# Kernel optimization log

Measured on AMD Instinct MI355X. Metric: run time of the kernel, lower is better.

The kernel has to match this reference:

```python
import jax, jax.numpy as jnp
import numpy as np

N = 4096
TAU = 0.2          # args.tau relaxation temperature
EPS = 1e-10        # numerical guard for logit of clamped probs


def setup_inputs() -> dict:
    key = jax.random.key(0)
    k1, k2, k3 = jax.random.split(key, 3)
    r = jax.random.uniform(k1, (N, N))
    ori_adj = jnp.where(r < 0.005, -1.0, jnp.where(r < 0.01, 1.0, 0.0)).astype(jnp.float32)
    # nn.init.uniform_(change_links_prob, 0.0, 0.001)
    change_links_prob = jax.random.uniform(k2, (N, N), minval=0.0, maxval=0.001, dtype=jnp.float32)
    # uniform noise for the RelaxedBernoulli logistic reparameterization
    u = jax.random.uniform(k3, (N, N), minval=1e-6, maxval=1.0 - 1e-6, dtype=jnp.float32)
    return {"ori_adj": ori_adj, "change_links_prob": change_links_prob, "u": u}


def reference(ori_adj, change_links_prob, u):
    # --- get_modified_adj: RelaxedBernoulliStraightThrough(tau, clamp(p,0,1)).rsample() ---
    p = jnp.clip(change_links_prob, EPS, 1.0 - EPS)      # torch.clamp(p, 0, 1) + logit guard
    logits = jnp.log(p) - jnp.log1p(-p)
    noise = jnp.log(u) - jnp.log1p(-u)                   # logistic noise
    soft = jax.nn.sigmoid((logits + noise) / TAU)        # relaxed sample
    hard = jnp.round(soft)                               # quantized sample
    change_prob = soft + jax.lax.stop_gradient(hard - soft)  # straight-through
    mod_adj = ori_adj + change_prob * (-2.0 * ori_adj)   # ori_adj * (1 - 2*b)

    # --- balance_degree_directed(mod_adj) ---
    # torch.diag(matrix) returns the diagonal VECTOR, broadcast-subtracted per row (faithful).
    A = mod_adj + mod_adj.T - jnp.diag(mod_adj)
    A_abs = jnp.abs(A)
    tr3 = jnp.einsum('ij,jk,ki->', A, A, A)              # trace(A @ A @ A)
    tr3_abs = jnp.einsum('ij,jk,ki->', A_abs, A_abs, A_abs)
    balance = 0.5 * (1.0 + tr3 / tr3_abs)
    return mod_adj, balance
```

## Files before the change

kernel.cpp:

```cpp
#include <hip/hip_runtime.h>
#include <hip/hip_bf16.h>
#include <cstdint>
#include <cstddef>

#define N 4096
#define NN ((size_t)N * (size_t)N)

typedef int int4v  __attribute__((ext_vector_type(4)));
typedef int int16v __attribute__((ext_vector_type(16)));

__device__ inline void async16(const void* g, void* lds) {
    __builtin_amdgcn_global_load_lds(
        (const __attribute__((address_space(1))) void*)g,
        (__attribute__((address_space(3))) void*)lds, 16, 0, 0);
}

__device__ inline float mod_elem(float p, float uu, float o) {
    p = fminf(fmaxf(p, 1e-10f), 1.0f - 1e-10f);
    float logits = logf(p) - log1pf(-p);
    float noise  = logf(uu) - log1pf(-uu);
    float y = (logits + noise) / 0.2f;
    float soft = 1.0f / (1.0f + expf(-y));
    float hard = rintf(soft);
    return o + hard * (-2.0f * o);
}

__global__ void diag_kernel(const float* __restrict__ ori, const float* __restrict__ clp,
                            const float* __restrict__ u, float* __restrict__ diag,
                            double* __restrict__ accs) {
    int j = blockIdx.x * blockDim.x + threadIdx.x;
    size_t idx = (size_t)j * N + j;
    diag[j] = mod_elem(clp[idx], u[idx], ori[idx]);
    if (blockIdx.x == 0 && threadIdx.x < 2) accs[threadIdx.x] = 0.0;
}

__global__ __launch_bounds__(256) void fused_mod_A(
        const float* __restrict__ ori, const float* __restrict__ clp,
        const float* __restrict__ u, const float* __restrict__ diag,
        float* __restrict__ out,
        signed char* __restrict__ A, signed char* __restrict__ AT,
        signed char* __restrict__ Aa, signed char* __restrict__ ATa) {
    const int bx = blockIdx.x, by = blockIdx.y;
    if (bx > by) return;
    const int bi = bx * 32, bj = by * 32;
    __shared__ float mij[32][33];
    __shared__ float mji[32][33];
    const int t = threadIdx.x;
    const int r  = t >> 3;
    const int c4 = (t & 7) * 4;
    {
        size_t idx = (size_t)(bi + r) * N + bj + c4;
        float4 p4 = *(const float4*)&clp[idx];
        float4 u4 = *(const float4*)&u[idx];
        float4 o4 = *(const float4*)&ori[idx];
        float m0 = mod_elem(p4.x, u4.x, o4.x);
        float m1 = mod_elem(p4.y, u4.y, o4.y);
        float m2 = mod_elem(p4.z, u4.z, o4.z);
        float m3 = mod_elem(p4.w, u4.w, o4.w);
        *(float4*)&out[idx] = make_float4(m0, m1, m2, m3);
        mij[r][c4] = m0; mij[r][c4 + 1] = m1; mij[r][c4 + 2] = m2; mij[r][c4 + 3] = m3;
        if (bx != by) {
            size_t idx2 = (size_t)(bj + r) * N + bi + c4;
            float4 q4 = *(const float4*)&clp[idx2];
            float4 v4 = *(const float4*)&u[idx2];
            float4 w4 = *(const float4*)&ori[idx2];
            float n0 = mod_elem(q4.x, v4.x, w4.x);
            float n1 = mod_elem(q4.y, v4.y, w4.y);
            float n2 = mod_elem(q4.z, v4.z, w4.z);
            float n3 = mod_elem(q4.w, v4.w, w4.w);
            *(float4*)&out[idx2] = make_float4(n0, n1, n2, n3);
            mji[r][c4] = n0; mji[r][c4 + 1] = n1; mji[r][c4 + 2] = n2; mji[r][c4 + 3] = n3;
        } else {
            mji[r][c4] = m0; mji[r][c4 + 1] = m1; mji[r][c4 + 2] = m2; mji[r][c4 + 3] = m3;
        }
    }
    __syncthreads();
    const float djr = diag[bj + r];
    const float dir = diag[bi + r];
    int pkA = 0, pkAa = 0, pkT = 0, pkTa = 0;
    int qkA = 0, qkAa = 0, qkT = 0, qkTa = 0;
    #pragma unroll
    for (int k = 0; k < 4; ++k) {
        const int c = c4 + k;
        const float x = mij[r][c], xt = mij[c][r];
        const float y = mji[r][c], yt = mji[c][r];
        int ai = (int)(x + yt - diag[bj + c]);
        int ti = (int)(xt + y - djr);
        pkA  |= (ai & 255) << (8 * k);
        pkAa |= ((ai < 0 ? -ai : ai) & 255) << (8 * k);
        pkT  |= (ti & 255) << (8 * k);
        pkTa |= ((ti < 0 ? -ti : ti) & 255) << (8 * k);
        int mi = (int)(y + xt - diag[bi + c]);
        int si = (int)(yt + x - dir);
        qkA  |= (mi & 255) << (8 * k);
        qkAa |= ((mi < 0 ? -mi : mi) & 255) << (8 * k);
        qkT  |= (si & 255) << (8 * k);
        qkTa |= ((si < 0 ? -si : si) & 255) << (8 * k);
    }
    const size_t o1 = (size_t)(bi + r) * N + bj + c4;
    const size_t o2 = (size_t)(bj + r) * N + bi + c4;
    *(int*)&A [o1] = pkA;  *(int*)&Aa [o1] = pkAa;
    *(int*)&AT[o2] = pkT;  *(int*)&ATa[o2] = pkTa;
    if (bx != by) {
        *(int*)&A [o2] = qkA;  *(int*)&Aa [o2] = qkAa;
        *(int*)&AT[o1] = qkT;  *(int*)&ATa[o1] = qkTa;
    }
}

__global__ __launch_bounds__(256) void gemm_trace_i8(const signed char* __restrict__ Ag,
                                                     const signed char* __restrict__ ATg,
                                                     const signed char* __restrict__ Aag,
                                                     const signed char* __restrict__ ATag,
                                                     double* __restrict__ accs) {
    __shared__ int4v As4[1024];
    __shared__ int4v Bs4[1024];
    __shared__ int red[4];
    const int z = blockIdx.z;
    const signed char* Asrc = z ? Aag  : Ag;
    const signed char* Bsrc = z ? ATag : ATg;
    const int i0 = blockIdx.y * 128;
    const int k0 = blockIdx.x * 128;
    const int t = threadIdx.x;
    const int lane = t & 63;
    const int wave = t >> 6;
    const int wr = (wave >> 1) * 64;
    const int wc = (wave & 1) * 64;
    const int m32 = lane & 31;
    const int kg  = lane >> 5;
    signed char* Asc = (signed char*)As4;
    signed char* Bsc = (signed char*)Bs4;

    const int r0 = t >> 2;
    const int c0 = (t & 3) ^ ((r0 >> 1) & 3);
    const signed char* gA = Asrc + (size_t)(i0 + r0) * N + c0 * 16;
    const signed char* gB = Bsrc + (size_t)(k0 + r0) * N + c0 * 16;
    const int ldst = t * 16;

    int16v acc[2][2];
    #pragma unroll
    for (int a = 0; a < 2; ++a)
        #pragma unroll
        for (int b = 0; b < 2; ++b)
            acc[a][b] = (int16v)(0);

    for (int kb = 0; kb < N; kb += 128) {
        __syncthreads();
        const signed char* ga = gA + kb;
        const signed char* gb = gB + kb;
        async16(ga,               Asc + ldst);
        async16(ga + 64 * N,      Asc + 4096  + ldst);
        async16(ga + 64,          Asc + 8192  + ldst);
        async16(ga + 64 * N + 64, Asc + 12288 + ldst);
        async16(gb,               Bsc + ldst);
        async16(gb + 64 * N,      Bsc + 4096  + ldst);
        async16(gb + 64,          Bsc + 8192  + ldst);
        async16(gb + 64 * N + 64, Bsc + 12288 + ldst);
        __syncthreads();
        #pragma unroll
        for (int half = 0; half < 2; ++half) {
            const int hb = half * 8192;
            #pragma unroll
            for (int q = 0; q < 2; ++q) {
                int4v af[2], bf[2];
                #pragma unroll
                for (int tr = 0; tr < 2; ++tr) {
                    const int row = wr + tr * 32 + m32;
                    const int slot = (q * 2 + kg) ^ ((row >> 1) & 3);
                    af[tr] = *(const int4v*)(Asc + hb + (row << 6) + (slot << 4));
                }
                #pragma unroll
                for (int tc = 0; tc < 2; ++tc) {
                    const int row = wc + tc * 32 + m32;
                    const int slot = (q * 2 + kg) ^ ((row >> 1) & 3);
                    bf[tc] = *(const int4v*)(Bsc + hb + (row << 6) + (slot << 4));
                }
                #pragma unroll
                for (int tr = 0; tr < 2; ++tr)
                    #pragma unroll
                    for (int tc = 0; tc < 2; ++tc)
                        acc[tr][tc] = __builtin_amdgcn_mfma_i32_32x32x32_i8(
                            af[tr], bf[tc], acc[tr][tc], 0, 0, 0);
            }
        }
    }

    int part = 0;
    const int rbase = 4 * kg;
    #pragma unroll
    for (int tr = 0; tr < 2; ++tr) {
        #pragma unroll
        for (int tc = 0; tc < 2; ++tc) {
            const int ib = i0 + wr + tr * 32;
            const int kk = k0 + wc + tc * 32 + m32;
            #pragma unroll
            for (int reg = 0; reg < 16; ++reg) {
                const int row = (reg & 3) + 8 * (reg >> 2) + rbase;
                part += acc[tr][tc][reg] * (int)Bsrc[(size_t)(ib + row) * N + kk];
            }
        }
    }
    #pragma unroll
    for (int off = 32; off > 0; off >>= 1)
        part += __shfl_down(part, off, 64);
    if (lane == 0) red[wave] = part;
    __syncthreads();
    if (t == 0) {
        int tot = red[0] + red[1] + red[2] + red[3];
        atomicAdd(&accs[z], (double)tot);
    }
}

__global__ void finalize_kernel(const double* __restrict__ accs, float* __restrict__ out) {
    out[NN] = (float)(0.5 * (1.0 + accs[0] / accs[1]));
}

extern "C" void kernel_launch(void* const* d_in, const int* in_sizes, int n_in,
                              void* d_out, int out_size, void* d_ws, size_t ws_size,
                              hipStream_t stream) {
    const float* ori = (const float*)d_in[0];
    const float* clp = (const float*)d_in[1];
    const float* u   = (const float*)d_in[2];
    float* out = (float*)d_out;
    char* ws = (char*)d_ws;
    signed char* A8   = (signed char*)ws;
    signed char* AT8  = (signed char*)(ws + NN);
    signed char* Aa8  = (signed char*)(ws + 2 * NN);
    signed char* ATa8 = (signed char*)(ws + 3 * NN);
    float*       diag = (float*)(ws + 4 * NN);
    double*      accs = (double*)(ws + 4 * NN + 4096 * 4);

    diag_kernel<<<dim3(16), 256, 0, stream>>>(ori, clp, u, diag, accs);
    fused_mod_A<<<dim3(N / 32, N / 32), 256, 0, stream>>>(ori, clp, u, diag, out,
                                                          A8, AT8, Aa8, ATa8);
    gemm_trace_i8<<<dim3(N / 128, N / 128, 2), 256, 0, stream>>>(A8, AT8, Aa8, ATa8, accs);
    finalize_kernel<<<1, 1, 0, stream>>>(accs, out);
}
```

Baseline: 448.7 us.

## Replace sampling transcendentals with threshold test and enlarge transpose tile to 64

The sigmoid/logit/log-noise chain is replaced by a direct comparison: hard=1 exactly when p+u>1, since the rounding of sigmoid((logit p + logit u)/tau) depends only on the sign of the argument. Only near-boundary cases fall back to the full transcendental path. The elementwise/transpose kernel also moves from 32x32 to 64x64 tiles, with diagonal values cached in LDS and 16-byte packed int8 stores. This removes most of the expensive log/exp work and cuts launch and grid overhead. It risks mismatches in rare borderline cases and raises LDS use per block.

```diff
diff --git a/kernel.cpp b/kernel.cpp
--- a/kernel.cpp
+++ b/kernel.cpp
@@ -15,14 +15,22 @@
         (__attribute__((address_space(3))) void*)lds, 16, 0, 0);
 }
 
-__device__ inline float mod_elem(float p, float uu, float o) {
-    p = fminf(fmaxf(p, 1e-10f), 1.0f - 1e-10f);
+__device__ __noinline__ float mod_full(float p_raw, float uu, float o) {
+    float p = fminf(fmaxf(p_raw, 1e-10f), 1.0f - 1e-10f);
     float logits = logf(p) - log1pf(-p);
     float noise  = logf(uu) - log1pf(-uu);
     float y = (logits + noise) / 0.2f;
     float soft = 1.0f / (1.0f + expf(-y));
     float hard = rintf(soft);
     return o + hard * (-2.0f * o);
+}
+
+__device__ inline float mod_elem(float p_raw, float uu, float o) {
+    float p = fmaxf(p_raw, 1e-10f);
+    float s = p + uu;
+    if (__builtin_expect(fabsf(s - 1.0f) < 1e-5f, 0))
+        return mod_full(p_raw, uu, o);
+    return (s > 1.0f) ? -o : o;
 }
 
 __global__ void diag_kernel(const float* __restrict__ ori, const float* __restrict__ clp,
@@ -32,6 +40,15 @@
     size_t idx = (size_t)j * N + j;
     diag[j] = mod_elem(clp[idx], u[idx], ori[idx]);
     if (blockIdx.x == 0 && threadIdx.x < 2) accs[threadIdx.x] = 0.0;
+}
+
+__device__ inline int pk4(const int* v) {
+    return (v[0] & 255) | ((v[1] & 255) << 8) | ((v[2] & 255) << 16) | ((v[3] & 255) << 24);
+}
+__device__ inline int pk4a(const int* v) {
+    int a0 = v[0] < 0 ? -v[0] : v[0], a1 = v[1] < 0 ? -v[1] : v[1];
+    int a2 = v[2] < 0 ? -v[2] : v[2], a3 = v[3] < 0 ? -v[3] : v[3];
+    return a0 | (a1 << 8) | (a2 << 16) | (a3 << 24);
 }
 
 __global__ __launch_bounds__(256) void fused_mod_A(
@@ -42,68 +59,79 @@
         signed char* __restrict__ Aa, signed char* __restrict__ ATa) {
     const int bx = blockIdx.x, by = blockIdx.y;
     if (bx > by) return;
-    const int bi = bx * 32, bj = by * 32;
-    __shared__ float mij[32][33];
-    __shared__ float mji[32][33];
+    const bool dg = (bx == by);
+    const int bi = bx * 64, bj = by * 64;
+    __shared__ float mij[64][68];
+    __shared__ float mji[64][68];
+    __shared__ float dj_s[64], di_s[64];
     const int t = threadIdx.x;
-    const int r  = t >> 3;
-    const int c4 = (t & 7) * 4;
+    const int r = t >> 2;
+    const int c16 = (t & 3) << 4;
+    if (t < 64) dj_s[t] = diag[bj + t];
+    else if (t < 128) di_s[t - 64] = diag[bi + t - 64];
     {
-        size_t idx = (size_t)(bi + r) * N + bj + c4;
-        float4 p4 = *(const float4*)&clp[idx];
-        float4 u4 = *(const float4*)&u[idx];
-        float4 o4 = *(const float4*)&ori[idx];
-        float m0 = mod_elem(p4.x, u4.x, o4.x);
-        float m1 = mod_elem(p4.y, u4.y, o4.y);
-        float m2 = mod_elem(p4.z, u4.z, o4.z);
-        float m3 = mod_elem(p4.w, u4.w, o4.w);
-        *(float4*)&out[idx] = make_float4(m0, m1, m2, m3);
-        mij[r][c4] = m0; mij[r][c4 + 1] = m1; mij[r][c4 + 2] = m2; mij[r][c4 + 3] = m3;
-        if (bx != by) {
-            size_t idx2 = (size_t)(bj + r) * N + bi + c4;
-            float4 q4 = *(const float4*)&clp[idx2];
-            float4 v4 = *(const float4*)&u[idx2];
-            float4 w4 = *(const float4*)&ori[idx2];
-            float n0 = mod_elem(q4.x, v4.x, w4.x);
-            float n1 = mod_elem(q4.y, v4.y, w4.y);
-            float n2 = mod_elem(q4.z, v4.z, w4.z);
-            float n3 = mod_elem(q4.w, v4.w, w4.w);
-            *(float4*)&out[idx2] = make_float4(n0, n1, n2, n3);
-            mji[r][c4] = n0; mji[r][c4 + 1] = n1; mji[r][c4 + 2] = n2; mji[r][c4 + 3] = n3;
-        } else {
-            mji[r][c4] = m0; mji[r][c4 + 1] = m1; mji[r][c4 + 2] = m2; mji[r][c4 + 3] = m3;
+        const size_t base = (size_t)(bi + r) * N + bj + c16;
+        #pragma unroll
+        for (int q = 0; q < 4; ++q) {
+            const size_t idx = base + q * 4;
+            float4 p4 = *(const float4*)&clp[idx];
+            float4 u4 = *(const float4*)&u[idx];
+            float4 o4 = *(const float4*)&ori[idx];
+            float4 m4;
+            m4.x = mod_elem(p4.x, u4.x, o4.x);
+            m4.y = mod_elem(p4.y, u4.y, o4.y);
+            m4.z = mod_elem(p4.z, u4.z, o4.z);
+            m4.w = mod_elem(p4.w, u4.w, o4.w);
+            *(float4*)&out[idx] = m4;
+            *(float4*)&mij[r][c16 + q * 4] = m4;
+        }
+    }
+    if (!dg) {
+        const size_t base = (size_t)(bj + r) * N + bi + c16;
+        #pragma unroll
+        for (int q = 0; q < 4; ++q) {
+            const size_t idx = base + q * 4;
+            float4 p4 = *(const float4*)&clp[idx];
+            float4 u4 = *(const float4*)&u[idx];
+            float4 o4 = *(const float4*)&ori[idx];
+            float4 m4;
+            m4.x = mod_elem(p4.x, u4.x, o4.x);
+            m4.y = mod_elem(p4.y, u4.y, o4.y);
+            m4.z = mod_elem(p4.z, u4.z, o4.z);
+            m4.w = mod_elem(p4.w, u4.w, o4.w);
+            *(float4*)&out[idx] = m4;
+            *(float4*)&mji[r][c16 + q * 4] = m4;
         }
     }
     __syncthreads();
-    const float djr = diag[bj + r];
-    const float dir = diag[bi + r];
-    int pkA = 0, pkAa = 0, pkT = 0, pkTa = 0;
-    int qkA = 0, qkAa = 0, qkT = 0, qkTa = 0;
-    #pragma unroll
-    for (int k = 0; k < 4; ++k) {
-        const int c = c4 + k;
-        const float x = mij[r][c], xt = mij[c][r];
-        const float y = mji[r][c], yt = mji[c][r];
-        int ai = (int)(x + yt - diag[bj + c]);
-        int ti = (int)(xt + y - djr);
-        pkA  |= (ai & 255) << (8 * k);
-        pkAa |= ((ai < 0 ? -ai : ai) & 255) << (8 * k);
-        pkT  |= (ti & 255) << (8 * k);
-        pkTa |= ((ti < 0 ? -ti : ti) & 255) << (8 * k);
-        int mi = (int)(y + xt - diag[bi + c]);
-        int si = (int)(yt + x - dir);
-        qkA  |= (mi & 255) << (8 * k);
-        qkAa |= ((mi < 0 ? -mi : mi) & 255) << (8 * k);
-        qkT  |= (si & 255) << (8 * k);
-        qkTa |= ((si < 0 ? -si : si) & 255) << (8 * k);
-    }
-    const size_t o1 = (size_t)(bi + r) * N + bj + c4;
-    const size_t o2 = (size_t)(bj + r) * N + bi + c4;
-    *(int*)&A [o1] = pkA;  *(int*)&Aa [o1] = pkAa;
-    *(int*)&AT[o2] = pkT;  *(int*)&ATa[o2] = pkTa;
-    if (bx != by) {
-        *(int*)&A [o2] = qkA;  *(int*)&Aa [o2] = qkAa;
-        *(int*)&AT[o1] = qkT;  *(int*)&ATa[o1] = qkTa;
+    float (*Mji)[68] = dg ? mij : mji;
+    int aF[16], tF[16], aM[16], tM[16];
+    const float djr = dj_s[r], dir = di_s[r];
+    #pragma unroll
+    for (int k = 0; k < 16; ++k) {
+        const int c = c16 + k;
+        const float x  = mij[r][c];
+        const float xt = mij[c][r];
+        const float y  = Mji[r][c];
+        const float yt = Mji[c][r];
+        aF[k] = (int)(x + yt - dj_s[c]);
+        tF[k] = (int)(xt + y - djr);
+        if (!dg) {
+            aM[k] = (int)(y + xt - di_s[c]);
+            tM[k] = (int)(yt + x - dir);
+        }
+    }
+    const size_t oF = (size_t)(bi + r) * N + bj + c16;
+    const size_t oM = (size_t)(bj + r) * N + bi + c16;
+    *(int4*)&A  [oF] = make_int4(pk4 (aF), pk4 (aF + 4), pk4 (aF + 8), pk4 (aF + 12));
+    *(int4*)&Aa [oF] = make_int4(pk4a(aF), pk4a(aF + 4), pk4a(aF + 8), pk4a(aF + 12));
+    *(int4*)&AT [oM] = make_int4(pk4 (tF), pk4 (tF + 4), pk4 (tF + 8), pk4 (tF + 12));
+    *(int4*)&ATa[oM] = make_int4(pk4a(tF), pk4a(tF + 4), pk4a(tF + 8), pk4a(tF + 12));
+    if (!dg) {
+        *(int4*)&A  [oM] = make_int4(pk4 (aM), pk4 (aM + 4), pk4 (aM + 8), pk4 (aM + 12));
+        *(int4*)&Aa [oM] = make_int4(pk4a(aM), pk4a(aM + 4), pk4a(aM + 8), pk4a(aM + 12));
+        *(int4*)&AT [oF] = make_int4(pk4 (tM), pk4 (tM + 4), pk4 (tM + 8), pk4 (tM + 12));
+        *(int4*)&ATa[oF] = make_int4(pk4a(tM), pk4a(tM + 4), pk4a(tM + 8), pk4a(tM + 12));
     }
 }
 
@@ -230,7 +258,7 @@
     double*      accs = (double*)(ws + 4 * NN + 4096 * 4);
 
     diag_kernel<<<dim3(16), 256, 0, stream>>>(ori, clp, u, diag, accs);
-    fused_mod_A<<<dim3(N / 32, N / 32), 256, 0, stream>>>(ori, clp, u, diag, out,
+    fused_mod_A<<<dim3(N / 64, N / 64), 256, 0, stream>>>(ori, clp, u, diag, out,
                                                           A8, AT8, Aa8, ATa8);
     gemm_trace_i8<<<dim3(N / 128, N / 128, 2), 256, 0, stream>>>(A8, AT8, Aa8, ATa8, accs);
     finalize_kernel<<<1, 1, 0, stream>>>(accs, out);
```

After: 451.9 us. About the same (+0.7%).
